# Optimization experiments

Measured on AMD Instinct MI355X. Metric: run time of the kernel, lower is better.

## Reference

```python
import jax, jax.numpy as jnp
import numpy as np

N = 4096  # number of nodes (matches fill_max of edge indices)


def _dense(edges, n):
    # edges: [2, E] int; dense {0,1} adjacency. Duplicate edges collapse (set semantics).
    return jnp.zeros((n, n), dtype=jnp.float32).at[edges[0], edges[1]].set(1.0)


def setup_inputs() -> dict:
    key = jax.random.key(0)
    ks = jax.random.split(key, 4)
    E = 200000
    mk = lambda k: jax.random.randint(k, (2, E), 0, N, dtype=jnp.int32)
    return {
        "A_pos_t": mk(ks[0]),
        "A_pos_tp1": mk(ks[1]),
        "A_neg_t": mk(ks[2]),
        "A_neg_tp1": mk(ks[3]),
    }


def reference(A_pos_t, A_pos_tp1, A_neg_t, A_neg_tp1):
    p_t = _dense(A_pos_t, N)
    p1 = _dense(A_pos_tp1, N)
    n_t = _dense(A_neg_t, N)
    n1 = _dense(A_neg_tp1, N)

    # edge_index_diff: set symmetric difference == elementwise xor of {0,1} adjacency
    xor_p = p_t + p1 - 2.0 * p_t * p1
    xor_n = n_t + n1 - 2.0 * n_t * n1

    # Balance theory triangle closure on (tp1) graphs.
    # sign(a,b): +1 if pos edge (pos checked first -> priority), -1 elif neg edge.
    sp = p1                      # positive-sign edge indicator
    sn = n1 * (1.0 - p1)         # negative-sign edge indicator (pos has priority)
    off = 1.0 - jnp.eye(N, dtype=jnp.float32)
    spo = sp * off               # exclude b==a / b==c (triples are distinct)
    sno = sn * off

    # number of 2-paths a->b->c with predicted sign +1 / -1
    M_same = spo @ spo + sno @ sno
    M_diff = spo @ sno + sno @ spo

    # the Python loop only infers edges (a,c) with a < c (orientations (i,j,k),(i,k,j),(j,i,k))
    tri = jnp.triu(jnp.ones((N, N), dtype=jnp.float32), k=1)

    ind_p = M_same * tri * (1.0 - p1)  # skip pairs already positively connected
    ind_n = M_diff * tri * (1.0 - n1)  # skip pairs already negatively connected

    # Output: [2, N, N]; entry = xor indicator + indirect-edge multiplicity count
    return jnp.stack([xor_p + ind_p, xor_n + ind_n])
```

## Files before the change

### kernel.cpp

```cpp
#include <hip/hip_runtime.h>


#define NN 4096
#define NW 128
#define MASK_BYTES ((size_t)NN * NW * 4)
#define MASK_WORDS ((size_t)NN * NW)

typedef unsigned int u32;
typedef __attribute__((ext_vector_type(4))) int int4v;
typedef __attribute__((ext_vector_type(4))) float f32x4;

__device__ __forceinline__ void gload_lds16(const char* g, char* l) {
    __builtin_amdgcn_global_load_lds(
        (const __attribute__((address_space(1))) void*)g,
        (__attribute__((address_space(3))) void*)l, 16, 0, 0);
}


__global__ void scatter_all(const int* __restrict__ e0, const int* __restrict__ e1,
                            const int* __restrict__ e2, const int* __restrict__ e3,
                            int E0, int E1, int E2, int E3,
                            u32* __restrict__ ws) {
    int i = blockIdx.x * blockDim.x + threadIdx.x;
    u32* Pt = ws + 0 * MASK_WORDS;
    u32* P1 = ws + 1 * MASK_WORDS;
    u32* Nt = ws + 2 * MASK_WORDS;
    u32* N1 = ws + 3 * MASK_WORDS;
    if (i < E0) { int r = e0[i], c = e0[i + E0];
        atomicOr(&Pt[r * NW + (c >> 5)], 1u << (c & 31)); }
    if (i < E1) { int r = e1[i], c = e1[i + E1];
        atomicOr(&P1[r * NW + (c >> 5)], 1u << (c & 31)); }
    if (i < E2) { int r = e2[i], c = e2[i + E2];
        atomicOr(&Nt[r * NW + (c >> 5)], 1u << (c & 31)); }
    if (i < E3) { int r = e3[i], c = e3[i + E3];
        atomicOr(&N1[r * NW + (c >> 5)], 1u << (c & 31)); }
}

__device__ __forceinline__ int4v expand_e(u32 sp, u32 sn) {
    int4v E;
    #pragma unroll
    for (int i = 0; i < 4; i++) {
        u32 p = (((sp >> (4 * i)) & 0xFu) * 0x00204081u) & 0x01010101u;
        u32 n = (((sn >> (4 * i)) & 0xFu) * 0x00204081u) & 0x01010101u;
        E[i] = (int)(p | (n << 5));
    }
    return E;
}

__global__ void build_both(const u32* __restrict__ masks,
                           char* __restrict__ E, char* __restrict__ ET) {
    const u32* P  = masks + 1 * MASK_WORDS;
    const u32* Nm = masks + 3 * MASK_WORDS;
    if (blockIdx.x < 2048) {
        int w = blockIdx.x * 256 + threadIdx.x;
        u32 p = P[w];
        u32 n = Nm[w] & ~p;
        int a = w >> 7, col = w & 127;
        if ((a >> 5) == col) {
            u32 db = 1u << (a & 31);
            p &= ~db; n &= ~db;
        }
        char* dst = E + (size_t)a * NN + col * 32;
        *reinterpret_cast<int4v*>(dst)      = expand_e(p & 0xFFFFu, n & 0xFFFFu);
        *reinterpret_cast<int4v*>(dst + 16) = expand_e(p >> 16, n >> 16);
    } else {
        int gw = (blockIdx.x - 2048) * 4 + (threadIdx.x >> 6);
        int lane = threadIdx.x & 63;
        int ab = gw >> 7;
        int wc = gw & 127;
        u32 pw = P[(ab * 64 + lane) * NW + wc];
        u32 nw = Nm[(ab * 64 + lane) * NW + wc];
        u32 myp = 0, myn = 0;
        #pragma unroll
        for (int j = 0; j < 32; j++) {
            unsigned long long bp = __ballot((pw >> j) & 1u);
            unsigned long long bn = __ballot((nw >> j) & 1u);
            if ((lane & 31) == j) {
                myp = (lane < 32) ? (u32)bp : (u32)(bp >> 32);
                myn = (lane < 32) ? (u32)bn : (u32)(bn >> 32);
            }
        }
        u32 p = myp;
        u32 n = myn & ~p;
        int c = wc * 32 + (lane & 31);
        int abase = ab * 64 + (lane >> 5) * 32;
        if (c >= abase && c < abase + 32) {
            u32 db = 1u << (c - abase);
            p &= ~db; n &= ~db;
        }
        char* dst = ET + (size_t)c * NN + abase;
        *reinterpret_cast<int4v*>(dst)      = expand_e(p & 0xFFFFu, n & 0xFFFFu);
        *reinterpret_cast<int4v*>(dst + 16) = expand_e(p >> 16, n >> 16);
    }
}

__global__ __launch_bounds__(256, 2) void gemm_ep(
    const char* __restrict__ E, const char* __restrict__ ET,
    const u32* __restrict__ Pt, const u32* __restrict__ P1,
    const u32* __restrict__ Nt, const u32* __restrict__ N1,
    float* __restrict__ out)
{
    const int tid = threadIdx.x;
    const size_t plane = (size_t)NN * NN;

    int s_ = ((int)blockIdx.x & 7) * 66 + ((int)blockIdx.x >> 3);
    int by = (int)((65.0f - sqrtf(4225.0f - 8.0f * (float)s_)) * 0.5f);
    if (by > 31) by = 31;
    while (by > 0 && 32 * by - (by * (by - 1)) / 2 > s_) --by;
    while (32 * (by + 1) - ((by + 1) * by) / 2 <= s_) ++by;
    int bx = by + s_ - (32 * by - (by * (by - 1)) / 2);
    const int a0 = by << 7, c0 = bx << 7;

    __shared__ char LB[2][2][16384];

    const int wave = tid >> 6, lane = tid & 63;
    const int wr = (wave >> 1) * 64, wcol = (wave & 1) * 64;
    const int lr = lane & 15, lg = lane >> 4;

    const int srow = tid >> 3;
    const int sslot = tid & 7;
    const int soff = ((sslot ^ (srow & 7)) << 4);
    const char* gA0 = E  + (size_t)(a0 + srow)      * NN + soff;
    const char* gA1 = E  + (size_t)(a0 + 32 + srow) * NN + soff;
    const char* gA2 = E  + (size_t)(a0 + 64 + srow) * NN + soff;
    const char* gA3 = E  + (size_t)(a0 + 96 + srow) * NN + soff;
    const char* gB0 = ET + (size_t)(c0 + srow)      * NN + soff;
    const char* gB1 = ET + (size_t)(c0 + 32 + srow) * NN + soff;
    const char* gB2 = ET + (size_t)(c0 + 64 + srow) * NN + soff;
    const char* gB3 = ET + (size_t)(c0 + 96 + srow) * NN + soff;
    const int t16 = tid * 16;

    int4v acc[4][4];
    int4v zero = {0, 0, 0, 0};
    #pragma unroll
    for (int m = 0; m < 4; m++)
        #pragma unroll
        for (int n = 0; n < 4; n++) acc[m][n] = zero;

    #define STAGE(b, p)                                           \
        do {                                                      \
            const int koff = (p) * 128;                           \
            gload_lds16(gA0 + koff, &LB[b][0][t16]);              \
            gload_lds16(gA1 + koff, &LB[b][0][4096 + t16]);       \
            gload_lds16(gA2 + koff, &LB[b][0][8192 + t16]);       \
            gload_lds16(gA3 + koff, &LB[b][0][12288 + t16]);      \
            gload_lds16(gB0 + koff, &LB[b][1][t16]);              \
            gload_lds16(gB1 + koff, &LB[b][1][4096 + t16]);       \
            gload_lds16(gB2 + koff, &LB[b][1][8192 + t16]);       \
            gload_lds16(gB3 + koff, &LB[b][1][12288 + t16]);      \
        } while (0)

    #define COMPUTE(b)                                                          \
        do {                                                                    \
            _Pragma("unroll")                                                   \
            for (int ks = 0; ks < 2; ks++) {                                    \
                int4v bf[4];                                                    \
                _Pragma("unroll")                                               \
                for (int n = 0; n < 4; n++) {                                   \
                    int rowb = wcol + n * 16 + lr;                              \
                    bf[n] = *reinterpret_cast<const int4v*>(&LB[b][1][          \
                        rowb * 128 + (((ks * 4 + lg) ^ (rowb & 7)) << 4)]);     \
                }                                                               \
                __builtin_amdgcn_s_setprio(1);                                  \
                _Pragma("unroll")                                               \
                for (int m = 0; m < 4; m++) {                                   \
                    int rowa = wr + m * 16 + lr;                                \
                    int4v af = *reinterpret_cast<const int4v*>(&LB[b][0][       \
                        rowa * 128 + (((ks * 4 + lg) ^ (rowa & 7)) << 4)]);     \
                    _Pragma("unroll")                                           \
                    for (int n = 0; n < 4; n++)                                 \
                        acc[m][n] = __builtin_amdgcn_mfma_i32_16x16x64_i8(      \
                            af, bf[n], acc[m][n], 0, 0, 0);                     \
                }                                                               \
                __builtin_amdgcn_s_setprio(0);                                  \
            }                                                                   \
        } while (0)

    if (by != bx) {
        #pragma unroll 4
        for (int pass = 0; pass < 16; ++pass) {
            int e = pass * 1024 + tid * 4;
            int r = e >> 7, cc = e & 127;
            int widx = (c0 + r) * NW + ((a0 + cc) >> 5);
            int sh = cc & 31;
            u32 xp = (P1[widx] ^ Pt[widx]) >> sh;
            u32 xn = (N1[widx] ^ Nt[widx]) >> sh;
            f32x4 o0, o1;
            #pragma unroll
            for (int i = 0; i < 4; i++) {
                o0[i] = (float)((xp >> i) & 1u);
                o1[i] = (float)((xn >> i) & 1u);
            }
            size_t ob = (size_t)(c0 + r) * NN + a0 + cc;
            *reinterpret_cast<f32x4*>(out + ob) = o0;
            *reinterpret_cast<f32x4*>(out + plane + ob) = o1;
        }
    }

    STAGE(0, 0);
    asm volatile("s_waitcnt vmcnt(0)" ::: "memory");
    __builtin_amdgcn_s_barrier();

    int cur = 0;
    for (int p = 0; p < 31; ++p) {
        STAGE(cur ^ 1, p + 1);
        COMPUTE(cur);
        asm volatile("s_waitcnt vmcnt(0)" ::: "memory");
        __builtin_amdgcn_s_barrier();
        cur ^= 1;
    }
    COMPUTE(cur);
    #undef STAGE
    #undef COMPUTE

    #pragma unroll
    for (int m = 0; m < 4; m++) {
        #pragma unroll
        for (int n = 0; n < 4; n++) {
            #pragma unroll
            for (int q = 0; q < 4; q++) {
                int a = a0 + wr + m * 16 + lg * 4 + q;
                int c = c0 + wcol + n * 16 + lr;
                int widx = a * NW + (c >> 5);
                int bit = c & 31;
                u32 p1 = (P1[widx] >> bit) & 1u;
                u32 n1 = (N1[widx] >> bit) & 1u;
                u32 pt = (Pt[widx] >> bit) & 1u;
                u32 nt = (Nt[widx] >> bit) & 1u;
                int av = acc[m][n][q];
                int Ms = (av & 31) + (av >> 10);
                int Md = (av >> 5) & 31;
                int o0 = (int)(pt ^ p1) + ((a < c && !p1) ? Ms : 0);
                int o1 = (int)(nt ^ n1) + ((a < c && !n1) ? Md : 0);
                size_t oi = (size_t)a * NN + c;
                out[oi] = (float)o0;
                out[plane + oi] = (float)o1;
            }
        }
    }
}

extern "C" void kernel_launch(void* const* d_in, const int* in_sizes, int n_in,
                              void* d_out, int out_size, void* d_ws, size_t ws_size,
                              hipStream_t stream) {
    char* ws = (char*)d_ws;
    u32* masks = (u32*)ws;
    u32* Pt = masks + 0 * MASK_WORDS;
    u32* P1 = masks + 1 * MASK_WORDS;
    u32* Nt = masks + 2 * MASK_WORDS;
    u32* N1 = masks + 3 * MASK_WORDS;
    char* E  = ws + 4 * MASK_BYTES;
    char* ET = E + (size_t)NN * NN;

    hipMemsetAsync(d_ws, 0, 4 * MASK_BYTES, stream);

    int E0 = in_sizes[0] / 2, E1 = in_sizes[1] / 2;
    int E2 = in_sizes[2] / 2, E3 = in_sizes[3] / 2;
    int Emax = max(max(E0, E1), max(E2, E3));
    scatter_all<<<(Emax + 255) / 256, 256, 0, stream>>>(
        (const int*)d_in[0], (const int*)d_in[1], (const int*)d_in[2],
        (const int*)d_in[3], E0, E1, E2, E3, masks);

    build_both<<<4096, 256, 0, stream>>>(masks, E, ET);

    gemm_ep<<<528, 256, 0, stream>>>(E, ET, Pt, P1, Nt, N1, (float*)d_out);
}
```

Before: 131.8 us.

## Load A operand directly to registers in MFMA fragment layout, bypass LDS

Build the A operand (E) in a pre-swizzled layout that matches the MFMA fragment order, so each lane can load its fragments straight from global memory into registers. Only B now passes through LDS, which halves the shared memory footprint and allows raising launch bounds to 3 blocks per CU. The main loop is unrolled by two with register double-buffering of the A fragments and a partial vmcnt wait. The hipMemsetAsync is replaced by a custom zeroing kernel. The trade-offs are higher register pressure and uncoalesced-per-lane but contiguous 16B global loads for A, plus more build_both blocks.

```diff
diff --git a/kernel.cpp b/kernel.cpp
--- a/kernel.cpp
+++ b/kernel.cpp
@@ -16,6 +16,10 @@
         (__attribute__((address_space(3))) void*)l, 16, 0, 0);
 }
 
+
+__global__ void zero_ws(int4v* __restrict__ p) {
+    p[blockIdx.x * 256 + threadIdx.x] = int4v{0, 0, 0, 0};
+}
 
 __global__ void scatter_all(const int* __restrict__ e0, const int* __restrict__ e1,
                             const int* __restrict__ e2, const int* __restrict__ e3,
@@ -48,23 +52,11 @@
 }
 
 __global__ void build_both(const u32* __restrict__ masks,
-                           char* __restrict__ E, char* __restrict__ ET) {
+                           char* __restrict__ EA, char* __restrict__ ET) {
     const u32* P  = masks + 1 * MASK_WORDS;
     const u32* Nm = masks + 3 * MASK_WORDS;
     if (blockIdx.x < 2048) {
-        int w = blockIdx.x * 256 + threadIdx.x;
-        u32 p = P[w];
-        u32 n = Nm[w] & ~p;
-        int a = w >> 7, col = w & 127;
-        if ((a >> 5) == col) {
-            u32 db = 1u << (a & 31);
-            p &= ~db; n &= ~db;
-        }
-        char* dst = E + (size_t)a * NN + col * 32;
-        *reinterpret_cast<int4v*>(dst)      = expand_e(p & 0xFFFFu, n & 0xFFFFu);
-        *reinterpret_cast<int4v*>(dst + 16) = expand_e(p >> 16, n >> 16);
-    } else {
-        int gw = (blockIdx.x - 2048) * 4 + (threadIdx.x >> 6);
+        int gw = blockIdx.x * 4 + (threadIdx.x >> 6);
         int lane = threadIdx.x & 63;
         int ab = gw >> 7;
         int wc = gw & 127;
@@ -91,11 +83,26 @@
         char* dst = ET + (size_t)c * NN + abase;
         *reinterpret_cast<int4v*>(dst)      = expand_e(p & 0xFFFFu, n & 0xFFFFu);
         *reinterpret_cast<int4v*>(dst + 16) = expand_e(p >> 16, n >> 16);
-    }
-}
-
-__global__ __launch_bounds__(256, 2) void gemm_ep(
-    const char* __restrict__ E, const char* __restrict__ ET,
+    } else {
+        int v = (blockIdx.x - 2048) * 256 + threadIdx.x;
+        int a  = ((v >> 12) << 4) | (v & 15);
+        int kc = (v >> 4) & 255;
+        int wi = a * NW + (kc >> 1);
+        u32 p = P[wi];
+        u32 n = Nm[wi] & ~p;
+        int sh = (kc & 1) * 16;
+        u32 sp = (p >> sh) & 0xFFFFu;
+        u32 sn = (n >> sh) & 0xFFFFu;
+        if (kc == (a >> 4)) {
+            u32 db = 1u << (a & 15);
+            sp &= ~db; sn &= ~db;
+        }
+        *reinterpret_cast<int4v*>(EA + (size_t)v * 16) = expand_e(sp, sn);
+    }
+}
+
+__global__ __launch_bounds__(256, 3) void gemm_ep(
+    const char* __restrict__ EA, const char* __restrict__ ET,
     const u32* __restrict__ Pt, const u32* __restrict__ P1,
     const u32* __restrict__ Nt, const u32* __restrict__ N1,
     float* __restrict__ out)
@@ -111,24 +118,21 @@
     int bx = by + s_ - (32 * by - (by * (by - 1)) / 2);
     const int a0 = by << 7, c0 = bx << 7;
 
-    __shared__ char LB[2][2][16384];
+    __shared__ char LB[2][16384];
 
     const int wave = tid >> 6, lane = tid & 63;
     const int wr = (wave >> 1) * 64, wcol = (wave & 1) * 64;
     const int lr = lane & 15, lg = lane >> 4;
 
-    const int srow = tid >> 3;
-    const int sslot = tid & 7;
+    const int srow = tid >> 3, sslot = tid & 7;
     const int soff = ((sslot ^ (srow & 7)) << 4);
-    const char* gA0 = E  + (size_t)(a0 + srow)      * NN + soff;
-    const char* gA1 = E  + (size_t)(a0 + 32 + srow) * NN + soff;
-    const char* gA2 = E  + (size_t)(a0 + 64 + srow) * NN + soff;
-    const char* gA3 = E  + (size_t)(a0 + 96 + srow) * NN + soff;
     const char* gB0 = ET + (size_t)(c0 + srow)      * NN + soff;
     const char* gB1 = ET + (size_t)(c0 + 32 + srow) * NN + soff;
     const char* gB2 = ET + (size_t)(c0 + 64 + srow) * NN + soff;
     const char* gB3 = ET + (size_t)(c0 + 96 + srow) * NN + soff;
     const int t16 = tid * 16;
+
+    const char* bA = EA + ((size_t)((a0 + wr) >> 4) << 16) + (lg << 8) + lr * 16;
 
     int4v acc[4][4];
     int4v zero = {0, 0, 0, 0};
@@ -137,20 +141,29 @@
         #pragma unroll
         for (int n = 0; n < 4; n++) acc[m][n] = zero;
 
-    #define STAGE(b, p)                                           \
+    int4v aX[8], aY[8];
+
+    #define STAGE_B(b, p)                                         \
         do {                                                      \
             const int koff = (p) * 128;                           \
-            gload_lds16(gA0 + koff, &LB[b][0][t16]);              \
-            gload_lds16(gA1 + koff, &LB[b][0][4096 + t16]);       \
-            gload_lds16(gA2 + koff, &LB[b][0][8192 + t16]);       \
-            gload_lds16(gA3 + koff, &LB[b][0][12288 + t16]);      \
-            gload_lds16(gB0 + koff, &LB[b][1][t16]);              \
-            gload_lds16(gB1 + koff, &LB[b][1][4096 + t16]);       \
-            gload_lds16(gB2 + koff, &LB[b][1][8192 + t16]);       \
-            gload_lds16(gB3 + koff, &LB[b][1][12288 + t16]);      \
+            gload_lds16(gB0 + koff, &LB[b][t16]);                 \
+            gload_lds16(gB1 + koff, &LB[b][4096 + t16]);          \
+            gload_lds16(gB2 + koff, &LB[b][8192 + t16]);          \
+            gload_lds16(gB3 + koff, &LB[b][12288 + t16]);         \
         } while (0)
 
-    #define COMPUTE(b)                                                          \
+    #define ALOAD(A, p)                                                        \
+        do {                                                                   \
+            _Pragma("unroll")                                                  \
+            for (int m = 0; m < 4; m++) {                                      \
+                A[m * 2]     = *reinterpret_cast<const int4v*>(                \
+                    bA + m * 65536 + (p) * 2048);                              \
+                A[m * 2 + 1] = *reinterpret_cast<const int4v*>(                \
+                    bA + m * 65536 + (p) * 2048 + 1024);                       \
+            }                                                                  \
+        } while (0)
+
+    #define COMPUTE(b, A)                                                       \
         do {                                                                    \
             _Pragma("unroll")                                                   \
             for (int ks = 0; ks < 2; ks++) {                                    \
@@ -158,19 +171,16 @@
                 _Pragma("unroll")                                               \
                 for (int n = 0; n < 4; n++) {                                   \
                     int rowb = wcol + n * 16 + lr;                              \
-                    bf[n] = *reinterpret_cast<const int4v*>(&LB[b][1][          \
+                    bf[n] = *reinterpret_cast<const int4v*>(&LB[b][             \
                         rowb * 128 + (((ks * 4 + lg) ^ (rowb & 7)) << 4)]);     \
                 }                                                               \
                 __builtin_amdgcn_s_setprio(1);                                  \
                 _Pragma("unroll")                                               \
                 for (int m = 0; m < 4; m++) {                                   \
-                    int rowa = wr + m * 16 + lr;                                \
-                    int4v af = *reinterpret_cast<const int4v*>(&LB[b][0][       \
-                        rowa * 128 + (((ks * 4 + lg) ^ (rowa & 7)) << 4)]);     \
                     _Pragma("unroll")                                           \
                     for (int n = 0; n < 4; n++)                                 \
                         acc[m][n] = __builtin_amdgcn_mfma_i32_16x16x64_i8(      \
-                            af, bf[n], acc[m][n], 0, 0, 0);                     \
+                            A[m * 2 + ks], bf[n], acc[m][n], 0, 0, 0);          \
                 }                                                               \
                 __builtin_amdgcn_s_setprio(0);                                  \
             }                                                                   \
@@ -197,20 +207,35 @@
         }
     }
 
-    STAGE(0, 0);
-    asm volatile("s_waitcnt vmcnt(0)" ::: "memory");
+    STAGE_B(0, 0);
+    __builtin_amdgcn_sched_barrier(0);
+    ALOAD(aX, 0);
+    asm volatile("s_waitcnt vmcnt(8)" ::: "memory");
     __builtin_amdgcn_s_barrier();
 
-    int cur = 0;
-    for (int p = 0; p < 31; ++p) {
-        STAGE(cur ^ 1, p + 1);
-        COMPUTE(cur);
-        asm volatile("s_waitcnt vmcnt(0)" ::: "memory");
+    for (int p = 0; p < 30; p += 2) {
+        STAGE_B(1, p + 1);
+        __builtin_amdgcn_sched_barrier(0);
+        ALOAD(aY, p + 1);
+        COMPUTE(0, aX);
+        asm volatile("s_waitcnt vmcnt(8)" ::: "memory");
         __builtin_amdgcn_s_barrier();
-        cur ^= 1;
-    }
-    COMPUTE(cur);
-    #undef STAGE
+        STAGE_B(0, p + 2);
+        __builtin_amdgcn_sched_barrier(0);
+        ALOAD(aX, p + 2);
+        COMPUTE(1, aY);
+        asm volatile("s_waitcnt vmcnt(8)" ::: "memory");
+        __builtin_amdgcn_s_barrier();
+    }
+    STAGE_B(1, 31);
+    __builtin_amdgcn_sched_barrier(0);
+    ALOAD(aY, 31);
+    COMPUTE(0, aX);
+    asm volatile("s_waitcnt vmcnt(8)" ::: "memory");
+    __builtin_amdgcn_s_barrier();
+    COMPUTE(1, aY);
+    #undef STAGE_B
+    #undef ALOAD
     #undef COMPUTE
 
     #pragma unroll
@@ -249,10 +274,10 @@
     u32* P1 = masks + 1 * MASK_WORDS;
     u32* Nt = masks + 2 * MASK_WORDS;
     u32* N1 = masks + 3 * MASK_WORDS;
-    char* E  = ws + 4 * MASK_BYTES;
-    char* ET = E + (size_t)NN * NN;
-
-    hipMemsetAsync(d_ws, 0, 4 * MASK_BYTES, stream);
+    char* EA = ws + 4 * MASK_BYTES;
+    char* ET = EA + (size_t)NN * NN;
+
+    zero_ws<<<2048, 256, 0, stream>>>((int4v*)masks);
 
     int E0 = in_sizes[0] / 2, E1 = in_sizes[1] / 2;
     int E2 = in_sizes[2] / 2, E3 = in_sizes[3] / 2;
@@ -261,7 +286,7 @@
         (const int*)d_in[0], (const int*)d_in[1], (const int*)d_in[2],
         (const int*)d_in[3], E0, E1, E2, E3, masks);
 
-    build_both<<<4096, 256, 0, stream>>>(masks, E, ET);
-
-    gemm_ep<<<528, 256, 0, stream>>>(E, ET, Pt, P1, Nt, N1, (float*)d_out);
-}
+    build_both<<<6144, 256, 0, stream>>>(masks, EA, ET);
+
+    gemm_ep<<<528, 256, 0, stream>>>(EA, ET, Pt, P1, Nt, N1, (float*)d_out);
+}
```

After: 144.8 us. 1.1x slower.
